# Kernel optimization log

Measured on AMD Instinct MI355X. Metric: run time of the kernel, lower is better.

## Reference

```python
import jax, jax.numpy as jnp
import numpy as np

B, M, D, P, T = 512, 16, 128, 16, 4096
GAMMA = 1.0  # similarity_size


def setup_inputs() -> dict:
    key = jax.random.key(0)
    k1, k2, k3, k4, k5 = jax.random.split(key, 5)
    phi = jax.random.normal(k1, (B, P), dtype=jnp.float32)
    state = jax.random.normal(k2, (B, D), dtype=jnp.float32)
    trajectories = jax.random.normal(k3, (T, D), dtype=jnp.float32)
    # Stand-in per-model KAARMA state-transition parameters (linear recurrent + input map, tanh)
    A = jax.random.normal(k4, (M, D, D), dtype=jnp.float32) * (1.0 / np.sqrt(D))
    B_in = jax.random.normal(k5, (M, P, D), dtype=jnp.float32) * (1.0 / np.sqrt(P))
    return {"phi": phi, "state": state, "trajectories": trajectories, "A": A, "B_in": B_in}


def reference(phi, state, trajectories, A, B_in):
    # per-model state update: new_state[b,m,:] = tanh(state @ A_m + phi @ B_m)
    new_state = jnp.tanh(
        jnp.einsum("bd,mdh->bmh", state, A) + jnp.einsum("bp,mph->bmh", phi, B_in)
    )  # [B, M, D]
    # RBF similarity vs trajectory set via ||s||^2 + ||t||^2 - 2 s.t (single batched GEMM)
    s_sq = jnp.sum(new_state * new_state, axis=-1, keepdims=True)      # [B, M, 1]
    t_sq = jnp.sum(trajectories * trajectories, axis=-1)               # [T]
    cross = jnp.einsum("bmd,td->bmt", new_state, trajectories)         # [B, M, T]
    sq_dist = jnp.maximum(s_sq + t_sq[None, None, :] - 2.0 * cross, 0.0)
    sim = jnp.exp(-GAMMA * sq_dist)                                    # [B, M, T]
    output = sim.reshape(phi.shape[0], -1)                             # [B, M*T]
    return output, new_state
```

## Files before the change

### kernel.cpp

```cpp
#include <hip/hip_runtime.h>
#include <hip/hip_bf16.h>
#include <cstdint>
#include <cstddef>

#define NB 512
#define NM 16
#define ND 128
#define NP 16
#define NT 4096

typedef __bf16 bf16x8 __attribute__((ext_vector_type(8)));
typedef __bf16 bf16x4 __attribute__((ext_vector_type(4)));
typedef float f32x4 __attribute__((ext_vector_type(4)));

static_assert(sizeof(bf16x8) == 16, "bf16x8 must be 16B");

__device__ __forceinline__ void gload_lds16(const void* g, void* l) {
  __builtin_amdgcn_global_load_lds(
      (const __attribute__((address_space(1))) unsigned int*)g,
      (__attribute__((address_space(3))) unsigned int*)l, 16, 0, 0);
}

__global__ __launch_bounds__(256) void prep_kernel(
    const float* __restrict__ phi, const float* __restrict__ state,
    const float* __restrict__ traj, const float* __restrict__ A,
    const float* __restrict__ Bin, float* __restrict__ ns_out,
    __bf16* __restrict__ ns_bf, __bf16* __restrict__ tj_bf,
    float* __restrict__ s_sq, float* __restrict__ t_sq) {
  __shared__ float sA[128 * 128];
  __shared__ float sSt[16 * 128];
  __shared__ float sBin[16 * 128];
  __shared__ float sPhi[16 * 16];
  __shared__ float sRed[16 * 2];
  __shared__ float sPart[256];
  const int tid = threadIdx.x;
  const int bx = blockIdx.x;

  if (bx < 512) {
    const int m = bx & 15;
    const int b0 = (bx >> 4) * 16;
    const float4* A4 = (const float4*)(A + (size_t)m * 16384);
    float4* sA4 = (float4*)sA;
#pragma unroll
    for (int i = 0; i < 16; ++i) sA4[tid + i * 256] = A4[tid + i * 256];
    const float4* S4 = (const float4*)(state + (size_t)b0 * 128);
    float4* sSt4 = (float4*)sSt;
    sSt4[tid] = S4[tid];
    sSt4[tid + 256] = S4[tid + 256];
    const float4* B4 = (const float4*)(Bin + (size_t)m * 2048);
    float4* sBin4 = (float4*)sBin;
    sBin4[tid] = B4[tid];
    sBin4[tid + 256] = B4[tid + 256];
    sPhi[tid] = phi[b0 * 16 + tid];
    __syncthreads();

    const int h = tid & 127;
    const int rg = tid >> 7;
    float acc[8];
#pragma unroll
    for (int j = 0; j < 8; ++j) acc[j] = 0.f;
    const float4* st4 = (const float4*)sSt;
    for (int dd = 0; dd < 32; ++dd) {
      const float a0 = sA[(dd * 4 + 0) * 128 + h];
      const float a1 = sA[(dd * 4 + 1) * 128 + h];
      const float a2 = sA[(dd * 4 + 2) * 128 + h];
      const float a3 = sA[(dd * 4 + 3) * 128 + h];
#pragma unroll
      for (int j = 0; j < 8; ++j) {
        const float4 sv = st4[(rg * 8 + j) * 32 + dd];
        acc[j] = fmaf(sv.x, a0, acc[j]);
        acc[j] = fmaf(sv.y, a1, acc[j]);
        acc[j] = fmaf(sv.z, a2, acc[j]);
        acc[j] = fmaf(sv.w, a3, acc[j]);
      }
    }
#pragma unroll
    for (int p = 0; p < 16; ++p) {
      const float bv = sBin[p * 128 + h];
#pragma unroll
      for (int j = 0; j < 8; ++j)
        acc[j] = fmaf(sPhi[(rg * 8 + j) * 16 + p], bv, acc[j]);
    }

#pragma unroll
    for (int j = 0; j < 8; ++j) {
      const float v = tanhf(acc[j]);
      const int R = (b0 + rg * 8 + j) * 16 + m;
      ns_out[(size_t)R * 128 + h] = v;
      ns_bf[(size_t)R * 128 + h] = (__bf16)v;
      float s = v * v;
#pragma unroll
      for (int o = 32; o > 0; o >>= 1) s += __shfl_xor(s, o, 64);
      if ((tid & 63) == 0) sRed[(rg * 8 + j) * 2 + ((tid >> 6) & 1)] = s;
    }
    __syncthreads();
    if (tid < 16)
      s_sq[(b0 + tid) * 16 + m] = sRed[tid * 2] + sRed[tid * 2 + 1];
  } else {
    const int t0 = (bx - 512) * 128;
    const int row = t0 + (tid >> 1);
    const int half = tid & 1;
    const size_t base = (size_t)row * 128 + half * 64;
    const float4* T4 = (const float4*)traj;
    float s = 0.f;
#pragma unroll
    for (int i = 0; i < 16; ++i) {
      const float4 v = T4[base / 4 + i];
      s += v.x * v.x + v.y * v.y + v.z * v.z + v.w * v.w;
      bf16x4 o;
      o[0] = (__bf16)v.x;
      o[1] = (__bf16)v.y;
      o[2] = (__bf16)v.z;
      o[3] = (__bf16)v.w;
      *(bf16x4*)(tj_bf + base + i * 4) = o;
    }
    sPart[tid] = s;
    __syncthreads();
    if (tid < 128) t_sq[t0 + tid] = sPart[2 * tid] + sPart[2 * tid + 1];
  }
}

__global__ __launch_bounds__(256) void sim_kernel(
    const __bf16* __restrict__ ns_bf, const __bf16* __restrict__ tj_bf,
    const float* __restrict__ s_sq, const float* __restrict__ t_sq,
    float* __restrict__ out) {
  __shared__ alignas(16) __bf16 sA[128 * 128];
  __shared__ alignas(16) __bf16 sB[128 * 128];
  __shared__ float sSq[128];
  __shared__ float sTq[128];
  const int tid = threadIdx.x;
  const int lane = tid & 63;
  const int w = tid >> 6;
  const int R0 = blockIdx.x * 128;
  const int C0 = blockIdx.y * 128;

  const char* gA = (const char*)(ns_bf + (size_t)R0 * 128);
  const char* gB = (const char*)(tj_bf + (size_t)C0 * 128);
#pragma unroll
  for (int it = 0; it < 8; ++it) {
    const int off = it * 4096 + w * 1024;
    gload_lds16(gA + off + lane * 16, (char*)sA + off);
    gload_lds16(gB + off + lane * 16, (char*)sB + off);
  }
  if (tid < 128)
    sSq[tid] = s_sq[R0 + tid];
  else
    sTq[tid - 128] = t_sq[C0 + tid - 128];
  __syncthreads();

  const int rbase = (w >> 1) * 64;
  const int cbase = (w & 1) * 64;
  const int l15 = lane & 15;
  const int quad = lane >> 4;

  f32x4 acc[4][4];
#pragma unroll
  for (int i = 0; i < 4; ++i)
#pragma unroll
    for (int j = 0; j < 4; ++j) acc[i][j] = (f32x4){0.f, 0.f, 0.f, 0.f};

#pragma unroll
  for (int ks = 0; ks < 4; ++ks) {
    const int koff = quad * 8 + ks * 32;
    bf16x8 af[4], bf[4];
#pragma unroll
    for (int i = 0; i < 4; ++i)
      af[i] = *(const bf16x8*)&sA[(rbase + i * 16 + l15) * 128 + koff];
#pragma unroll
    for (int i = 0; i < 4; ++i)
      bf[i] = *(const bf16x8*)&sB[(cbase + i * 16 + l15) * 128 + koff];
#pragma unroll
    for (int ri = 0; ri < 4; ++ri)
#pragma unroll
      for (int ci = 0; ci < 4; ++ci)
        acc[ri][ci] = __builtin_amdgcn_mfma_f32_16x16x32_bf16(
            af[ri], bf[ci], acc[ri][ci], 0, 0, 0);
  }

#pragma unroll
  for (int ri = 0; ri < 4; ++ri) {
    const int rl = rbase + ri * 16 + quad * 4;
#pragma unroll
    for (int ci = 0; ci < 4; ++ci) {
      const int cl = cbase + ci * 16 + l15;
      const float tq = sTq[cl];
      const size_t col = (size_t)(C0 + cl);
#pragma unroll
      for (int r = 0; r < 4; ++r) {
        const float d0 = sSq[rl + r] + tq - 2.f * acc[ri][ci][r];
        const float d = fmaxf(d0, 0.f);
        out[(size_t)(R0 + rl + r) * NT + col] = expf(-d);
      }
    }
  }
}

extern "C" void kernel_launch(void* const* d_in, const int* in_sizes, int n_in,
                              void* d_out, int out_size, void* d_ws,
                              size_t ws_size, hipStream_t stream) {
  (void)in_sizes; (void)n_in; (void)out_size; (void)ws_size;
  const float* phi   = (const float*)d_in[0];
  const float* state = (const float*)d_in[1];
  const float* traj  = (const float*)d_in[2];
  const float* A     = (const float*)d_in[3];
  const float* Bin   = (const float*)d_in[4];

  float* out = (float*)d_out;
  float* out_ns = out + (size_t)NB * NM * NT;

  char* ws = (char*)d_ws;
  __bf16* ns_bf = (__bf16*)ws;
  __bf16* tj_bf = (__bf16*)(ws + (2u << 20));
  float* s_sq   = (float*)(ws + (3u << 20));
  float* t_sq   = (float*)(ws + (3u << 20) + (32u << 10));

  prep_kernel<<<544, 256, 0, stream>>>(phi, state, traj, A, Bin, out_ns, ns_bf,
                                       tj_bf, s_sq, t_sq);
  dim3 g2(NB * NM / 128, NT / 128);
  sim_kernel<<<g2, 256, 0, stream>>>(ns_bf, tj_bf, s_sq, t_sq, out);
}
```

Measured before the change: 183.5 us.

## Swizzle bf16 operand layout, transpose MFMA output for vector stores, stream A from global

The prep kernel now writes the bf16 state and trajectory tiles with an XOR swizzle on 16-byte chunks, and the sim kernel reads its LDS fragments with the matching swizzle to avoid bank conflicts. The MFMA operands are swapped so each lane holds four consecutive trajectory columns, which allows 16-byte vectorised output stores and uses the fast __expf. The prep GEMM no longer stages the 64KB A matrix in LDS; it reads A directly from global memory with a different thread mapping, which cuts LDS use but depends on cache hits for A. The bf16 conversion also moves to vector stores through a shared staging buffer.

```diff
diff --git a/kernel.cpp b/kernel.cpp
--- a/kernel.cpp
+++ b/kernel.cpp
@@ -10,7 +10,6 @@
 #define NT 4096
 
 typedef __bf16 bf16x8 __attribute__((ext_vector_type(8)));
-typedef __bf16 bf16x4 __attribute__((ext_vector_type(4)));
 typedef float f32x4 __attribute__((ext_vector_type(4)));
 
 static_assert(sizeof(bf16x8) == 16, "bf16x8 must be 16B");
@@ -27,96 +26,123 @@
     const float* __restrict__ Bin, float* __restrict__ ns_out,
     __bf16* __restrict__ ns_bf, __bf16* __restrict__ tj_bf,
     float* __restrict__ s_sq, float* __restrict__ t_sq) {
-  __shared__ float sA[128 * 128];
-  __shared__ float sSt[16 * 128];
-  __shared__ float sBin[16 * 128];
-  __shared__ float sPhi[16 * 16];
-  __shared__ float sRed[16 * 2];
-  __shared__ float sPart[256];
+  __shared__ alignas(16) float sSt[16 * 128];
+  __shared__ alignas(16) float sPhi[16 * 16];
+  __shared__ alignas(16) float sRes[16 * 128];
   const int tid = threadIdx.x;
   const int bx = blockIdx.x;
 
   if (bx < 512) {
     const int m = bx & 15;
     const int b0 = (bx >> 4) * 16;
-    const float4* A4 = (const float4*)(A + (size_t)m * 16384);
-    float4* sA4 = (float4*)sA;
-#pragma unroll
-    for (int i = 0; i < 16; ++i) sA4[tid + i * 256] = A4[tid + i * 256];
     const float4* S4 = (const float4*)(state + (size_t)b0 * 128);
     float4* sSt4 = (float4*)sSt;
     sSt4[tid] = S4[tid];
     sSt4[tid + 256] = S4[tid + 256];
-    const float4* B4 = (const float4*)(Bin + (size_t)m * 2048);
-    float4* sBin4 = (float4*)sBin;
-    sBin4[tid] = B4[tid];
-    sBin4[tid + 256] = B4[tid + 256];
     sPhi[tid] = phi[b0 * 16 + tid];
     __syncthreads();
 
-    const int h = tid & 127;
-    const int rg = tid >> 7;
-    float acc[8];
-#pragma unroll
-    for (int j = 0; j < 8; ++j) acc[j] = 0.f;
-    const float4* st4 = (const float4*)sSt;
-    for (int dd = 0; dd < 32; ++dd) {
-      const float a0 = sA[(dd * 4 + 0) * 128 + h];
-      const float a1 = sA[(dd * 4 + 1) * 128 + h];
-      const float a2 = sA[(dd * 4 + 2) * 128 + h];
-      const float a3 = sA[(dd * 4 + 3) * 128 + h];
-#pragma unroll
-      for (int j = 0; j < 8; ++j) {
-        const float4 sv = st4[(rg * 8 + j) * 32 + dd];
-        acc[j] = fmaf(sv.x, a0, acc[j]);
-        acc[j] = fmaf(sv.y, a1, acc[j]);
-        acc[j] = fmaf(sv.z, a2, acc[j]);
-        acc[j] = fmaf(sv.w, a3, acc[j]);
-      }
-    }
-#pragma unroll
-    for (int p = 0; p < 16; ++p) {
-      const float bv = sBin[p * 128 + h];
-#pragma unroll
-      for (int j = 0; j < 8; ++j)
-        acc[j] = fmaf(sPhi[(rg * 8 + j) * 16 + p], bv, acc[j]);
-    }
-
-#pragma unroll
-    for (int j = 0; j < 8; ++j) {
-      const float v = tanhf(acc[j]);
-      const int R = (b0 + rg * 8 + j) * 16 + m;
-      ns_out[(size_t)R * 128 + h] = v;
-      ns_bf[(size_t)R * 128 + h] = (__bf16)v;
-      float s = v * v;
-#pragma unroll
-      for (int o = 32; o > 0; o >>= 1) s += __shfl_xor(s, o, 64);
-      if ((tid & 63) == 0) sRed[(rg * 8 + j) * 2 + ((tid >> 6) & 1)] = s;
+    const int h2 = tid & 63;
+    const int rgrp = tid >> 6;
+    const float* Ap = A + (size_t)m * 16384 + h2;
+    const float* Bp = Bin + (size_t)m * 2048 + h2;
+
+    float acc[2][4];
+#pragma unroll
+    for (int hi = 0; hi < 2; ++hi)
+#pragma unroll
+      for (int j = 0; j < 4; ++j) acc[hi][j] = 0.f;
+
+#pragma unroll 4
+    for (int c = 0; c < 32; ++c) {
+      float a0[4], a1[4];
+#pragma unroll
+      for (int u = 0; u < 4; ++u) {
+        a0[u] = Ap[(size_t)(c * 4 + u) * 128];
+        a1[u] = Ap[(size_t)(c * 4 + u) * 128 + 64];
+      }
+#pragma unroll
+      for (int j = 0; j < 4; ++j) {
+        const f32x4 sv = *(const f32x4*)&sSt[(rgrp * 4 + j) * 128 + c * 4];
+#pragma unroll
+        for (int u = 0; u < 4; ++u) {
+          acc[0][j] = fmaf(sv[u], a0[u], acc[0][j]);
+          acc[1][j] = fmaf(sv[u], a1[u], acc[1][j]);
+        }
+      }
+    }
+#pragma unroll
+    for (int pc = 0; pc < 4; ++pc) {
+      float b0v[4], b1v[4];
+#pragma unroll
+      for (int u = 0; u < 4; ++u) {
+        b0v[u] = Bp[(size_t)(pc * 4 + u) * 128];
+        b1v[u] = Bp[(size_t)(pc * 4 + u) * 128 + 64];
+      }
+#pragma unroll
+      for (int j = 0; j < 4; ++j) {
+        const f32x4 pv = *(const f32x4*)&sPhi[(rgrp * 4 + j) * 16 + pc * 4];
+#pragma unroll
+        for (int u = 0; u < 4; ++u) {
+          acc[0][j] = fmaf(pv[u], b0v[u], acc[0][j]);
+          acc[1][j] = fmaf(pv[u], b1v[u], acc[1][j]);
+        }
+      }
+    }
+
+#pragma unroll
+    for (int j = 0; j < 4; ++j) {
+      const int row = rgrp * 4 + j;
+      const int R = (b0 + row) * 16 + m;
+      const float v0 = tanhf(acc[0][j]);
+      const float v1 = tanhf(acc[1][j]);
+      ns_out[(size_t)R * 128 + h2] = v0;
+      ns_out[(size_t)R * 128 + h2 + 64] = v1;
+      sRes[row * 128 + h2] = v0;
+      sRes[row * 128 + h2 + 64] = v1;
+      float s = v0 * v0 + v1 * v1;
+#pragma unroll
+      for (int o = 32; o > 0; o >>= 1) s += __shfl_xor(s, o);
+      if (h2 == 0) s_sq[R] = s;
     }
     __syncthreads();
-    if (tid < 16)
-      s_sq[(b0 + tid) * 16 + m] = sRed[tid * 2] + sRed[tid * 2 + 1];
+
+    {
+      const int row = tid >> 4;
+      const int kb = tid & 15;
+      const f32x4 r0 = *(const f32x4*)&sRes[row * 128 + kb * 8];
+      const f32x4 r1 = *(const f32x4*)&sRes[row * 128 + kb * 8 + 4];
+      bf16x8 o;
+#pragma unroll
+      for (int i = 0; i < 4; ++i) {
+        o[i] = (__bf16)r0[i];
+        o[i + 4] = (__bf16)r1[i];
+      }
+      const int R = (b0 + row) * 16 + m;
+      *(bf16x8*)(ns_bf + (size_t)R * 128 + ((kb ^ m) * 8)) = o;
+    }
   } else {
     const int t0 = (bx - 512) * 128;
-    const int row = t0 + (tid >> 1);
+    const int t = t0 + (tid >> 1);
     const int half = tid & 1;
-    const size_t base = (size_t)row * 128 + half * 64;
-    const float4* T4 = (const float4*)traj;
     float s = 0.f;
 #pragma unroll
-    for (int i = 0; i < 16; ++i) {
-      const float4 v = T4[base / 4 + i];
-      s += v.x * v.x + v.y * v.y + v.z * v.z + v.w * v.w;
-      bf16x4 o;
-      o[0] = (__bf16)v.x;
-      o[1] = (__bf16)v.y;
-      o[2] = (__bf16)v.z;
-      o[3] = (__bf16)v.w;
-      *(bf16x4*)(tj_bf + base + i * 4) = o;
-    }
-    sPart[tid] = s;
-    __syncthreads();
-    if (tid < 128) t_sq[t0 + tid] = sPart[2 * tid] + sPart[2 * tid + 1];
+    for (int q = 0; q < 8; ++q) {
+      const int kb = half * 8 + q;
+      const f32x4 v0 = *(const f32x4*)&traj[(size_t)t * 128 + kb * 8];
+      const f32x4 v1 = *(const f32x4*)&traj[(size_t)t * 128 + kb * 8 + 4];
+      s += v0[0] * v0[0] + v0[1] * v0[1] + v0[2] * v0[2] + v0[3] * v0[3];
+      s += v1[0] * v1[0] + v1[1] * v1[1] + v1[2] * v1[2] + v1[3] * v1[3];
+      bf16x8 o;
+#pragma unroll
+      for (int i = 0; i < 4; ++i) {
+        o[i] = (__bf16)v0[i];
+        o[i + 4] = (__bf16)v1[i];
+      }
+      *(bf16x8*)(tj_bf + (size_t)t * 128 + ((kb ^ (t & 15)) * 8)) = o;
+    }
+    s += __shfl_xor(s, 1);
+    if (half == 0) t_sq[t] = s;
   }
 }
 
@@ -161,36 +187,39 @@
 
 #pragma unroll
   for (int ks = 0; ks < 4; ++ks) {
-    const int koff = quad * 8 + ks * 32;
-    bf16x8 af[4], bf[4];
+    const int kb = quad + ks * 4;
+    const int koff = (kb ^ l15) * 8;
+    bf16x8 af[4], bfr[4];
 #pragma unroll
     for (int i = 0; i < 4; ++i)
       af[i] = *(const bf16x8*)&sA[(rbase + i * 16 + l15) * 128 + koff];
 #pragma unroll
     for (int i = 0; i < 4; ++i)
-      bf[i] = *(const bf16x8*)&sB[(cbase + i * 16 + l15) * 128 + koff];
+      bfr[i] = *(const bf16x8*)&sB[(cbase + i * 16 + l15) * 128 + koff];
 #pragma unroll
     for (int ri = 0; ri < 4; ++ri)
 #pragma unroll
       for (int ci = 0; ci < 4; ++ci)
         acc[ri][ci] = __builtin_amdgcn_mfma_f32_16x16x32_bf16(
-            af[ri], bf[ci], acc[ri][ci], 0, 0, 0);
+            bfr[ci], af[ri], acc[ri][ci], 0, 0, 0);
   }
 
 #pragma unroll
   for (int ri = 0; ri < 4; ++ri) {
-    const int rl = rbase + ri * 16 + quad * 4;
+    const int nsrow = rbase + ri * 16 + l15;
+    const float sq = sSq[nsrow];
+    float* orow = out + (size_t)(R0 + nsrow) * NT + C0;
 #pragma unroll
     for (int ci = 0; ci < 4; ++ci) {
-      const int cl = cbase + ci * 16 + l15;
-      const float tq = sTq[cl];
-      const size_t col = (size_t)(C0 + cl);
-#pragma unroll
-      for (int r = 0; r < 4; ++r) {
-        const float d0 = sSq[rl + r] + tq - 2.f * acc[ri][ci][r];
-        const float d = fmaxf(d0, 0.f);
-        out[(size_t)(R0 + rl + r) * NT + col] = expf(-d);
-      }
+      const int t4 = cbase + ci * 16 + quad * 4;
+      const f32x4 tq = *(const f32x4*)&sTq[t4];
+      f32x4 r;
+#pragma unroll
+      for (int k = 0; k < 4; ++k) {
+        const float d = fmaxf(sq + tq[k] - 2.f * acc[ri][ci][k], 0.f);
+        r[k] = __expf(-d);
+      }
+      *(f32x4*)&orow[t4] = r;
     }
   }
 }
```

Measured after the change: 168.7 us. 1.09x faster.
